# Performance work log

Measured on AMD Instinct MI355X. Metric: run time of the kernel, lower is better.

Reference implementation:

```python
import jax, jax.numpy as jnp
import numpy as np
from jax.scipy.special import logsumexp

N, M, D = 4096, 4096, 512
MASS = 0.9
REG = 0.1
REG_KL = 0.01
ITERS = 100


def setup_inputs() -> dict:
    key = jax.random.key(0)
    k0, k1 = jax.random.split(key)
    return {
        "ft0": jax.random.normal(k0, (N, D), dtype=jnp.float32),
        "ft1": jax.random.normal(k1, (M, D), dtype=jnp.float32),
        "bin_score": jnp.float32(0.4),
    }


def reference(ft0, ft1, bin_score):
    # all rows have norm >> 1e-8 for randn inputs -> foreground masks are all True
    f0 = ft0 / jnp.linalg.norm(ft0, axis=-1, keepdims=True)
    f1 = ft1 / jnp.linalg.norm(ft1, axis=-1, keepdims=True)
    cos_sim = f0 @ f1.T                       # [N, M]
    n, m = cos_sim.shape

    # partial OT marginals with dustbin mass (get_partial_distributions)
    a = jnp.concatenate([jnp.full((n,), MASS / n, jnp.float32),
                         jnp.array([1.0 - MASS], jnp.float32)])
    b = jnp.concatenate([jnp.full((m,), MASS / m, jnp.float32),
                         jnp.array([1.0 - MASS], jnp.float32)])
    log_mu, log_nu = jnp.log(a), jnp.log(b)   # [n+1], [m+1]

    # augment score matrix with dustbin row/col (get_partial_ot_problem)
    top = jnp.concatenate([cos_sim, jnp.broadcast_to(bin_score, (n, 1))], axis=1)
    bot = jnp.broadcast_to(bin_score, (1, m + 1))
    couplings = jnp.concatenate([top, bot], axis=0)   # [n+1, m+1]

    lmba = 1.0 / REG                         # = 10.0
    phi = REG_KL / (REG_KL + 1.0 / lmba)     # = 0.01 / 0.11
    Z = lmba * couplings

    def body(carry, _):
        u, v = carry
        u = (log_mu - logsumexp(Z + v[None, :] * lmba, axis=1)) / lmba * phi
        v = (log_nu - logsumexp(Z + u[:, None] * lmba, axis=0)) / lmba * phi
        return (u, v), None

    u0 = jnp.zeros((n + 1,), jnp.float32)
    v0 = jnp.zeros((m + 1,), jnp.float32)
    (u, v), _ = jax.lax.scan(body, (u0, v0), None, length=ITERS)

    prob = jnp.exp(Z + u[:, None] * lmba + v[None, :] * lmba)
    # prob_add_bkg with all-True masks: identity placement, zero the corner
    return prob.at[-1, -1].set(0.0)
```

## Files before the change

kernel.cpp:

```cpp
#include <hip/hip_runtime.h>
#include <math.h>

#define Nn 4096
#define Mm 4096
#define Dd 512
#define NP 4097
#define NPB 4104

#define PHI 0.09090909090909091f
#define LMU_IN  (-8.4231266823771690f)
#define LMU_BIN (-2.3025850929940457f)
#define LOG_NP  8.3180489582454150f

typedef __attribute__((ext_vector_type(8))) __bf16 bf16x8;
typedef __attribute__((ext_vector_type(4))) float  f32x4;

__device__ __forceinline__ void load_lds16(const __bf16* g, __bf16* l) {
    __builtin_amdgcn_global_load_lds(
        (__attribute__((address_space(1))) void*)g,
        (__attribute__((address_space(3))) void*)l,
        16, 0, 0);
}

__device__ __forceinline__ float block_allreduce_256(float v, float* sb) {
    #pragma unroll
    for (int off = 32; off > 0; off >>= 1) v += __shfl_down(v, off, 64);
    __syncthreads();
    if ((threadIdx.x & 63) == 0) sb[threadIdx.x >> 6] = v;
    __syncthreads();
    return sb[0] + sb[1] + sb[2] + sb[3];
}

__global__ __launch_bounds__(256) void normalize_bins_kernel(
    const float* __restrict__ F0, const float* __restrict__ F1,
    const float* __restrict__ binp,
    __bf16* __restrict__ A, __bf16* __restrict__ B, _Float16* __restrict__ Ef,
    float* __restrict__ S0, float* __restrict__ TcA) {
    __shared__ float sb[4];
    const int row = blockIdx.x;
    const float* src = (row < Nn) ? (F0 + (size_t)row * Dd)
                                  : (F1 + (size_t)(row - Nn) * Dd);
    __bf16* dst = (row < Nn) ? (A + (size_t)row * Dd)
                             : (B + (size_t)(row - Nn) * Dd);
    const float2 x = ((const float2*)src)[threadIdx.x];
    const float s = block_allreduce_256(x.x * x.x + x.y * x.y, sb);
    const float rn = rsqrtf(s);
    dst[2 * threadIdx.x]     = (__bf16)(x.x * rn);
    dst[2 * threadIdx.x + 1] = (__bf16)(x.y * rn);

    if (row < 17) {
        const int j = row * 256 + threadIdx.x;
        if (j < NP) Ef[(size_t)Nn * NPB + j] = (_Float16)__expf(10.0f * binp[0]);
    } else if (row < 33) {
        const int i = (row - 17) * 256 + threadIdx.x;
        Ef[(size_t)i * NPB + Mm] = (_Float16)__expf(10.0f * binp[0]);
    } else if (row < 50) {
        const int k = (row - 33) * 256 + threadIdx.x;
        if (k < NP) S0[k] = 0.f;
    } else if (row < 67) {
        const int k = (row - 50) * 256 + threadIdx.x;
        if (k < NP) TcA[k] = 0.f;
    }
}

#define BKq 32
#define CLD2 132
__global__ __launch_bounds__(256) void gemm_rowsum_kernel(
    const __bf16* __restrict__ A, const __bf16* __restrict__ B,
    _Float16* __restrict__ Ef, float* __restrict__ S0) {
    __shared__ __align__(16) __bf16 As[3][128 * BKq];
    __shared__ __align__(16) __bf16 Bs[3][128 * BKq];
    const int tid = threadIdx.x;
    const int l = tid & 63, wv = tid >> 6;
    const int wm = wv >> 1, wn = wv & 1;
    const int ln = l & 15, lq = l >> 4;

    const int bid = blockIdx.x;
    const int xcd = bid & 7, sub = bid >> 3;
    const int by = (xcd & 3) * 8 + (sub >> 4);
    const int bx = (xcd >> 2) * 16 + (sub & 15);
    const int row0 = by << 7, col0 = bx << 7;

    f32x4 acc[4][4];
    #pragma unroll
    for (int i = 0; i < 4; ++i)
        #pragma unroll
        for (int j = 0; j < 4; ++j) acc[i][j] = (f32x4){0.f, 0.f, 0.f, 0.f};

    const __bf16* aS[2]; const __bf16* bS[2]; int qE[2];
    #pragma unroll
    for (int p = 0; p < 2; ++p) {
        const int q = tid + p * 256;
        const int r = q >> 2, c = q & 3;
        const int cg = c ^ ((r >> 1) & 3);
        aS[p] = A + (size_t)(row0 + r) * Dd + cg * 8;
        bS[p] = B + (size_t)(col0 + r) * Dd + cg * 8;
        qE[p] = q * 8;
    }

    auto STAGE = [&](int b, int k0) {
        load_lds16(aS[0] + k0, &As[b][qE[0]]);
        load_lds16(aS[1] + k0, &As[b][qE[1]]);
        load_lds16(bS[0] + k0, &Bs[b][qE[0]]);
        load_lds16(bS[1] + k0, &Bs[b][qE[1]]);
    };

    #define WAITV(N) asm volatile("s_waitcnt vmcnt(" #N ")" ::: "memory")
    #define BAR() __builtin_amdgcn_s_barrier()

    const int sw = (ln >> 1) & 3;

    STAGE(0, 0); STAGE(1, BKq);
    WAITV(4); BAR();

    #pragma unroll
    for (int t = 0; t < 16; ++t) {
        const int buf = t % 3;
        if (t < 14) STAGE((t + 2) % 3, (t + 2) * BKq);
        bf16x8 bfr[4], af[4];
        #pragma unroll
        for (int ni = 0; ni < 4; ++ni)
            bfr[ni] = *(const bf16x8*)
                &Bs[buf][(wn * 64 + ni * 16 + ln) * BKq + (lq ^ sw) * 8];
        #pragma unroll
        for (int mi = 0; mi < 4; ++mi)
            af[mi] = *(const bf16x8*)
                &As[buf][(wm * 64 + mi * 16 + ln) * BKq + (lq ^ sw) * 8];
        __builtin_amdgcn_s_setprio(1);
        #pragma unroll
        for (int mi = 0; mi < 4; ++mi)
            #pragma unroll
            for (int ni = 0; ni < 4; ++ni)
                acc[mi][ni] = __builtin_amdgcn_mfma_f32_16x16x32_bf16(
                    af[mi], bfr[ni], acc[mi][ni], 0, 0, 0);
        __builtin_amdgcn_s_setprio(0);
        if (t < 14)      { WAITV(4); BAR(); }
        else if (t == 14){ WAITV(0); BAR(); }
    }
    #undef WAITV
    #undef BAR

    _Float16* Cs = (_Float16*)&As[0][0];
    #pragma unroll
    for (int p = 0; p < 2; ++p) {
        __syncthreads();
        #pragma unroll
        for (int m1 = 0; m1 < 2; ++m1) {
            const int mi = p * 2 + m1;
            #pragma unroll
            for (int r = 0; r < 4; ++r) {
                const int lr = wm * 32 + m1 * 16 + lq * 4 + r;
                float rs = 0.f;
                #pragma unroll
                for (int ni = 0; ni < 4; ++ni) {
                    const float e = __expf(10.0f * acc[mi][ni][r]);
                    Cs[lr * CLD2 + wn * 64 + ni * 16 + ln] = (_Float16)e;
                    rs += e;
                }
                rs += __shfl_down(rs, 8, 64);
                rs += __shfl_down(rs, 4, 64);
                rs += __shfl_down(rs, 2, 64);
                rs += __shfl_down(rs, 1, 64);
                if (ln == 0) {
                    const int gi = row0 + wm * 64 + mi * 16 + lq * 4 + r;
                    atomicAdd(&S0[gi], rs);
                }
            }
        }
        __syncthreads();
        #pragma unroll
        for (int pp = 0; pp < 4; ++pp) {
            const int q = tid + pp * 256;
            const int lr = q >> 4, ck = q & 15;
            const int gi = row0 + (lr >> 5) * 64 + p * 32 + (lr & 31);
            *(uint4*)(Ef + (size_t)gi * NPB + col0 + ck * 8) =
                *(const uint4*)&Cs[lr * CLD2 + ck * 8];
        }
    }
}

__global__ __launch_bounds__(256) void wvec_kernel(
    const float* __restrict__ Tc, float* __restrict__ W,
    float* __restrict__ Zero) {
    const int j = blockIdx.x * 256 + threadIdx.x;
    if (j < NP) {
        const float lnu = (j < Mm) ? LMU_IN : LMU_BIN;
        W[j] = __expf(PHI * (lnu - __logf(Tc[j])));
        if (Zero) Zero[j] = 0.f;
    }
}

__global__ __launch_bounds__(256) void col_pass_kernel(
    const _Float16* __restrict__ Ef, const float* __restrict__ S0,
    const float* __restrict__ eUarr, const float* __restrict__ binp,
    float* __restrict__ Tc, const int mode) {
    __shared__ float evl[128];
    const int tid = threadIdx.x;
    const int t = blockIdx.x;
    const int sI = blockIdx.y;
    const int r0 = sI * 128;

    if (tid < 128) {
        const int r = r0 + tid;
        float ev;
        if (mode == 0) {
            const float ebin = __expf(10.0f * binp[0]);
            ev = __expf(PHI * (LMU_IN - __logf(S0[r] + ebin)));
        } else {
            ev = eUarr[r];
        }
        evl[tid] = ev;
    }
    __syncthreads();

    const int j0 = t * 512 + tid * 2;
    const unsigned short* base = (const unsigned short*)Ef;
    float s0 = 0.f, s1 = 0.f;
    #pragma unroll 16
    for (int k = 0; k < 128; ++k) {
        const int r = r0 + k;
        union { unsigned u; _Float16 h[2]; } e;
        e.u = *(const unsigned*)(base + (size_t)r * NPB + j0);
        const float ev = evl[k];
        s0 += (float)e.h[0] * ev;
        s1 += (float)e.h[1] * ev;
    }

    float ev4096 = 0.f;
    if (sI == 31) {
        ev4096 = (mode == 0)
               ? __expf(PHI * (LMU_BIN - (LOG_NP + 10.0f * binp[0])))
               : eUarr[Nn];
        union { unsigned u; _Float16 h[2]; } e;
        e.u = *(const unsigned*)(base + (size_t)Nn * NPB + j0);
        s0 += (float)e.h[0] * ev4096;
        s1 += (float)e.h[1] * ev4096;
    }
    atomicAdd(&Tc[j0], s0);
    atomicAdd(&Tc[j0 + 1], s1);

    if (t == 0 && tid < 128) {
        float sc = (float)Ef[(size_t)(r0 + tid) * NPB + Mm] * evl[tid];
        if (sI == 31 && tid == 0)
            sc += (float)Ef[(size_t)Nn * NPB + Mm] * ev4096;
        #pragma unroll
        for (int off = 32; off > 0; off >>= 1) sc += __shfl_down(sc, off, 64);
        if ((tid & 63) == 0) atomicAdd(&Tc[Mm], sc);
    }
}

__global__ __launch_bounds__(256) void row_pass2_kernel(
    const _Float16* __restrict__ Ef, const float* __restrict__ W1,
    float* __restrict__ eU) {
    const int tid = threadIdx.x;
    const int wv = tid >> 6, l = tid & 63;
    const int i0 = blockIdx.x * 8;
    const float4* w4 = (const float4*)W1;

    #pragma unroll
    for (int k = 0; k < 2; ++k) {
        const int i = i0 + k * 4 + wv;
        if (i < NP) {
            const uint4* rowp = (const uint4*)(Ef + (size_t)i * NPB);
            float s = 0.f;
            #pragma unroll
            for (int c = 0; c < 8; ++c) {
                const int chunk = c * 64 + l;
                union { uint4 u; _Float16 h[8]; } e;
                e.u = rowp[chunk];
                const float4 w0 = w4[chunk * 2];
                const float4 w1 = w4[chunk * 2 + 1];
                s += (float)e.h[0] * w0.x + (float)e.h[1] * w0.y
                   + (float)e.h[2] * w0.z + (float)e.h[3] * w0.w
                   + (float)e.h[4] * w1.x + (float)e.h[5] * w1.y
                   + (float)e.h[6] * w1.z + (float)e.h[7] * w1.w;
            }
            if (l == 0) s += (float)Ef[(size_t)i * NPB + Mm] * W1[Mm];
            #pragma unroll
            for (int off = 32; off > 0; off >>= 1) s += __shfl_down(s, off, 64);
            if (l == 0) {
                const float lmu = (i < Nn) ? LMU_IN : LMU_BIN;
                eU[i] = __expf(PHI * (lmu - __logf(s)));
            }
        }
    }
}

__global__ __launch_bounds__(256) void finish_kernel(
    const _Float16* __restrict__ Ef, const float* __restrict__ eU,
    const float* __restrict__ W2, float* __restrict__ out) {
    __shared__ float wl[NP];
    const int tid = threadIdx.x;
    for (int c = tid; c < 1024; c += 256)
        ((float4*)wl)[c] = ((const float4*)W2)[c];
    if (tid == 0) wl[Mm] = W2[Mm];
    __syncthreads();

    const int i0 = blockIdx.x * 8;
    #pragma unroll 1
    for (int k = 0; k < 8; ++k) {
        const int i = i0 + k;
        if (i >= NP) break;
        const float sU = eU[i];
        const unsigned short* erow = (const unsigned short*)(Ef + (size_t)i * NPB);
        float* orow = out + (size_t)i * NP;
        #pragma unroll
        for (int c = 0; c < 16; ++c) {
            const int j = c * 256 + tid;
            union { unsigned short u; _Float16 h; } e;
            e.u = erow[j];
            orow[j] = (float)e.h * sU * wl[j];
        }
        if (tid == 0) {
            float v = (float)Ef[(size_t)i * NPB + Mm] * sU * wl[Mm];
            if (i == Nn) v = 0.f;
            orow[Mm] = v;
        }
    }
}


extern "C" void kernel_launch(void* const* d_in, const int* in_sizes, int n_in,
                              void* d_out, int out_size, void* d_ws, size_t ws_size,
                              hipStream_t stream) {
    const float* ft0 = (const float*)d_in[0];
    const float* ft1 = (const float*)d_in[1];
    const float* bin = (const float*)d_in[2];
    float* out = (float*)d_out;

    const size_t ABF_B = (size_t)Nn * Dd * 2;
    const size_t EBF_B = (size_t)NP * NPB * 2;
    const size_t VEC_B = 16400;
    __bf16*   Abf = (__bf16*)d_ws;
    __bf16*   Bbf = (__bf16*)((char*)d_ws + ABF_B);
    _Float16* Ef  = (_Float16*)((char*)d_ws + 2 * ABF_B);
    float*    eU  = (float*)((char*)d_ws + 2 * ABF_B + EBF_B);
    float*    S0  = (float*)((char*)d_ws + 2 * ABF_B + EBF_B + VEC_B);
    float*    TcA = (float*)((char*)d_ws + 2 * ABF_B + EBF_B + 2 * VEC_B);
    float*    TcB = (float*)((char*)d_ws + 2 * ABF_B + EBF_B + 3 * VEC_B);
    float*    W1  = (float*)((char*)d_ws + 2 * ABF_B + EBF_B + 4 * VEC_B);
    float*    W2  = (float*)((char*)d_ws + 2 * ABF_B + EBF_B + 5 * VEC_B);

    normalize_bins_kernel<<<Nn + Mm, 256, 0, stream>>>(ft0, ft1, bin,
                                                       Abf, Bbf, Ef, S0, TcA);
    gemm_rowsum_kernel<<<1024, 256, 0, stream>>>(Abf, Bbf, Ef, S0);
    col_pass_kernel<<<dim3(8, 32), 256, 0, stream>>>(Ef, S0, eU, bin, TcA, 0);
    wvec_kernel<<<17, 256, 0, stream>>>(TcA, W1, TcB);
    row_pass2_kernel<<<513, 256, 0, stream>>>(Ef, W1, eU);
    col_pass_kernel<<<dim3(8, 32), 256, 0, stream>>>(Ef, S0, eU, bin, TcB, 1);
    wvec_kernel<<<17, 256, 0, stream>>>(TcB, W2, nullptr);
    finish_kernel<<<513, 256, 0, stream>>>(Ef, eU, W2, out);
}
```

Baseline: 187.7 us.

## Enlarge GEMM tile to 256x128 with double-buffered LDS and half the blocks

The GEMM+rowsum kernel now computes a 256x128 output tile per block instead of 128x128. Each wave holds 8x4 MFMA accumulators, which raises B-operand reuse and halves the grid to 512 blocks. The triple-buffered async LDS pipeline with explicit vmcnt waits becomes a simpler double buffer with __syncthreads. The larger register footprint and fewer blocks may reduce occupancy and latency hiding, and the weaker pipelining could expose load latency.

Result: faster. 179.0 us (-4.7%).

```diff
diff --git a/kernel.cpp b/kernel.cpp
--- a/kernel.cpp
+++ b/kernel.cpp
@@ -64,12 +64,12 @@
 }
 
 #define BKq 32
-#define CLD2 132
-__global__ __launch_bounds__(256) void gemm_rowsum_kernel(
+#define CLD3 136
+__global__ __launch_bounds__(256, 2) void gemm_rowsum_kernel(
     const __bf16* __restrict__ A, const __bf16* __restrict__ B,
     _Float16* __restrict__ Ef, float* __restrict__ S0) {
-    __shared__ __align__(16) __bf16 As[3][128 * BKq];
-    __shared__ __align__(16) __bf16 Bs[3][128 * BKq];
+    __shared__ __align__(16) __bf16 As[2][256 * BKq];
+    __shared__ __align__(16) __bf16 Bs[2][128 * BKq];
     const int tid = threadIdx.x;
     const int l = tid & 63, wv = tid >> 6;
     const int wm = wv >> 1, wn = wv & 1;
@@ -77,72 +77,78 @@
 
     const int bid = blockIdx.x;
     const int xcd = bid & 7, sub = bid >> 3;
-    const int by = (xcd & 3) * 8 + (sub >> 4);
+    const int by = (xcd & 3) * 4 + (sub >> 4);
     const int bx = (xcd >> 2) * 16 + (sub & 15);
-    const int row0 = by << 7, col0 = bx << 7;
-
-    f32x4 acc[4][4];
-    #pragma unroll
-    for (int i = 0; i < 4; ++i)
+    const int row0 = by << 8, col0 = bx << 7;
+
+    f32x4 acc[8][4];
+    #pragma unroll
+    for (int i = 0; i < 8; ++i)
         #pragma unroll
         for (int j = 0; j < 4; ++j) acc[i][j] = (f32x4){0.f, 0.f, 0.f, 0.f};
 
-    const __bf16* aS[2]; const __bf16* bS[2]; int qE[2];
+    const __bf16* aS[4]; int qA[4];
+    #pragma unroll
+    for (int p = 0; p < 4; ++p) {
+        const int q = tid + p * 256;
+        const int r = q >> 2, c = q & 3;
+        const int cg = c ^ ((r >> 1) & 3);
+        aS[p] = A + (size_t)(row0 + r) * Dd + cg * 8;
+        qA[p] = q * 8;
+    }
+    const __bf16* bS[2]; int qB[2];
     #pragma unroll
     for (int p = 0; p < 2; ++p) {
         const int q = tid + p * 256;
         const int r = q >> 2, c = q & 3;
         const int cg = c ^ ((r >> 1) & 3);
-        aS[p] = A + (size_t)(row0 + r) * Dd + cg * 8;
         bS[p] = B + (size_t)(col0 + r) * Dd + cg * 8;
-        qE[p] = q * 8;
+        qB[p] = q * 8;
     }
 
     auto STAGE = [&](int b, int k0) {
-        load_lds16(aS[0] + k0, &As[b][qE[0]]);
-        load_lds16(aS[1] + k0, &As[b][qE[1]]);
-        load_lds16(bS[0] + k0, &Bs[b][qE[0]]);
-        load_lds16(bS[1] + k0, &Bs[b][qE[1]]);
+        #pragma unroll
+        for (int p = 0; p < 4; ++p) load_lds16(aS[p] + k0, &As[b][qA[p]]);
+        #pragma unroll
+        for (int p = 0; p < 2; ++p) load_lds16(bS[p] + k0, &Bs[b][qB[p]]);
     };
 
-    #define WAITV(N) asm volatile("s_waitcnt vmcnt(" #N ")" ::: "memory")
-    #define BAR() __builtin_amdgcn_s_barrier()
-
     const int sw = (ln >> 1) & 3;
 
-    STAGE(0, 0); STAGE(1, BKq);
-    WAITV(4); BAR();
-
-    #pragma unroll
+    STAGE(0, 0);
+    __syncthreads();
+    int buf = 0;
     for (int t = 0; t < 16; ++t) {
-        const int buf = t % 3;
-        if (t < 14) STAGE((t + 2) % 3, (t + 2) * BKq);
-        bf16x8 bfr[4], af[4];
+        if (t < 15) STAGE(buf ^ 1, (t + 1) * BKq);
+        bf16x8 bfr[4];
         #pragma unroll
         for (int ni = 0; ni < 4; ++ni)
             bfr[ni] = *(const bf16x8*)
-                &Bs[buf][(wn * 64 + ni * 16 + ln) * BKq + (lq ^ sw) * 8];
-        #pragma unroll
-        for (int mi = 0; mi < 4; ++mi)
-            af[mi] = *(const bf16x8*)
-                &As[buf][(wm * 64 + mi * 16 + ln) * BKq + (lq ^ sw) * 8];
+                &Bs[buf][(wn * 64 + ni * 16 + ln) * BKq + ((lq ^ sw) * 8)];
         __builtin_amdgcn_s_setprio(1);
         #pragma unroll
-        for (int mi = 0; mi < 4; ++mi)
-            #pragma unroll
-            for (int ni = 0; ni < 4; ++ni)
-                acc[mi][ni] = __builtin_amdgcn_mfma_f32_16x16x32_bf16(
-                    af[mi], bfr[ni], acc[mi][ni], 0, 0, 0);
+        for (int h = 0; h < 2; ++h) {
+            bf16x8 af[4];
+            #pragma unroll
+            for (int i = 0; i < 4; ++i)
+                af[i] = *(const bf16x8*)
+                    &As[buf][(wm * 128 + h * 64 + i * 16 + ln) * BKq
+                             + ((lq ^ sw) * 8)];
+            #pragma unroll
+            for (int i = 0; i < 4; ++i)
+                #pragma unroll
+                for (int ni = 0; ni < 4; ++ni)
+                    acc[h * 4 + i][ni] = __builtin_amdgcn_mfma_f32_16x16x32_bf16(
+                        af[i], bfr[ni], acc[h * 4 + i][ni], 0, 0, 0);
+        }
         __builtin_amdgcn_s_setprio(0);
-        if (t < 14)      { WAITV(4); BAR(); }
-        else if (t == 14){ WAITV(0); BAR(); }
-    }
-    #undef WAITV
-    #undef BAR
+        __syncthreads();
+        buf ^= 1;
+    }
 
     _Float16* Cs = (_Float16*)&As[0][0];
     #pragma unroll
-    for (int p = 0; p < 2; ++p) {
+    for (int p = 0; p < 4; ++p) {
         __syncthreads();
         #pragma unroll
         for (int m1 = 0; m1 < 2; ++m1) {
@@ -154,7 +160,7 @@
                 #pragma unroll
                 for (int ni = 0; ni < 4; ++ni) {
                     const float e = __expf(10.0f * acc[mi][ni][r]);
-                    Cs[lr * CLD2 + wn * 64 + ni * 16 + ln] = (_Float16)e;
+                    Cs[lr * CLD3 + wn * 64 + ni * 16 + ln] = (_Float16)e;
                     rs += e;
                 }
                 rs += __shfl_down(rs, 8, 64);
@@ -162,7 +168,7 @@
                 rs += __shfl_down(rs, 2, 64);
                 rs += __shfl_down(rs, 1, 64);
                 if (ln == 0) {
-                    const int gi = row0 + wm * 64 + mi * 16 + lq * 4 + r;
+                    const int gi = row0 + wm * 128 + mi * 16 + lq * 4 + r;
                     atomicAdd(&S0[gi], rs);
                 }
             }
@@ -172,9 +178,9 @@
         for (int pp = 0; pp < 4; ++pp) {
             const int q = tid + pp * 256;
             const int lr = q >> 4, ck = q & 15;
-            const int gi = row0 + (lr >> 5) * 64 + p * 32 + (lr & 31);
+            const int gi = row0 + (lr >> 5) * 128 + p * 32 + (lr & 31);
             *(uint4*)(Ef + (size_t)gi * NPB + col0 + ck * 8) =
-                *(const uint4*)&Cs[lr * CLD2 + ck * 8];
+                *(const uint4*)&Cs[lr * CLD3 + ck * 8];
         }
     }
 }
@@ -343,7 +349,7 @@
 
     normalize_bins_kernel<<<Nn + Mm, 256, 0, stream>>>(ft0, ft1, bin,
                                                        Abf, Bbf, Ef, S0, TcA);
-    gemm_rowsum_kernel<<<1024, 256, 0, stream>>>(Abf, Bbf, Ef, S0);
+    gemm_rowsum_kernel<<<512, 256, 0, stream>>>(Abf, Bbf, Ef, S0);
     col_pass_kernel<<<dim3(8, 32), 256, 0, stream>>>(Ef, S0, eU, bin, TcA, 0);
     wvec_kernel<<<17, 256, 0, stream>>>(TcA, W1, TcB);
     row_pass2_kernel<<<513, 256, 0, stream>>>(Ef, W1, eU);
```
